# Optimization experiments

Hardware: AMD Instinct MI355X
Metric: run time of the kernel (lower is better)

## Reference

```python
import jax, jax.numpy as jnp
import numpy as np

COL_IDX = 5  # colIdx: column used as sort key
REVERSE = False


def setup_inputs() -> dict:
    key = jax.random.key(0)
    # x: [batch, seq, feat]
    x = jax.random.normal(key, (32, 4096, 256), dtype=jnp.float32)
    return {"x": x}


def reference(x):
    # tf.nn.top_k(x[:, :, nc], k=S) returns indices of a full descending sort
    # with stable tie-breaking (earlier index first). jnp.argsort is stable,
    # so argsort of the negated key reproduces it exactly.
    keys = x[:, :, COL_IDX]                       # [B, S]
    idxs = jnp.argsort(-keys, axis=1)             # [B, S] descending order
    if REVERSE:
        idxs = idxs[:, ::-1]
    # gather_nd with (batch, idx) pairs == take_along_axis over the seq dim
    return jnp.take_along_axis(x, idxs[:, :, None], axis=1)  # [B, S, F]
```

## Files before the change

kernel.cpp:

```cpp
#include <hip/hip_runtime.h>
#include <stdint.h>

#define BATCH   32
#define ROWS    4096
#define COLS    256
#define COL_IDX 5

__global__ __launch_bounds__(1024)
void sort_keys_kernel(const float* __restrict__ x, int* __restrict__ idx_out) {
    __shared__ unsigned long long keys[ROWS];
    const int b = blockIdx.x;
    const float* xb = x + (size_t)b * ROWS * COLS;

    for (int i = threadIdx.x; i < ROWS; i += blockDim.x) {
        unsigned int u = __float_as_uint(xb[(size_t)i * COLS + COL_IDX]);
        u = (u >> 31) ? ~u : (u | 0x80000000u);
        u = ~u;
        keys[i] = ((unsigned long long)u << 32) | (unsigned int)i;
    }
    __syncthreads();

    for (int k = 2; k <= ROWS; k <<= 1) {
        for (int j = k >> 1; j > 0; j >>= 1) {
            for (int i = threadIdx.x; i < ROWS; i += blockDim.x) {
                int ixj = i ^ j;
                if (ixj > i) {
                    bool up = ((i & k) == 0);
                    unsigned long long a = keys[i];
                    unsigned long long c = keys[ixj];
                    if ((a > c) == up) { keys[i] = c; keys[ixj] = a; }
                }
            }
            __syncthreads();
        }
    }

    for (int i = threadIdx.x; i < ROWS; i += blockDim.x) {
        idx_out[b * ROWS + i] = (int)(keys[i] & 0xFFFFFFFFu);
    }
}

__global__ __launch_bounds__(256)
void gather_rows_kernel(const float* __restrict__ x,
                        const int* __restrict__ idx,
                        float* __restrict__ out) {
    const int r    = blockIdx.x * 4 + (threadIdx.x >> 6);
    const int lane = threadIdx.x & 63;
    const int b    = r >> 12;
    const int src  = idx[r];

    const float4* sp = (const float4*)(x   + ((size_t)b * ROWS + src) * COLS);
    float4*       dp = (float4*)      (out + (size_t)r * COLS);
    dp[lane] = sp[lane];
}

extern "C" void kernel_launch(void* const* d_in, const int* in_sizes, int n_in,
                              void* d_out, int out_size, void* d_ws, size_t ws_size,
                              hipStream_t stream) {
    const float* x   = (const float*)d_in[0];
    float*       out = (float*)d_out;
    int*         idx = (int*)d_ws;

    sort_keys_kernel<<<BATCH, 1024, 0, stream>>>(x, idx);
    gather_rows_kernel<<<(BATCH * ROWS) / 4, 256, 0, stream>>>(x, idx, out);
}
```

Baseline: 285.8 us.

## Replace per-batch bitonic sort with parallel rank counting and scatter copy

Swaps the single-block-per-batch bitonic sort in shared memory for a rank sort. One kernel extracts the packed keys with their row indices. A second kernel has each wavefront work out every row's rank by comparing against all 4096 keys through readlane broadcasts, then scatter each source row to its ranked output position. This spreads the sort over far more wavefronts instead of 32 blocks with many barriers, at the cost of O(N^2) comparisons per batch.

```diff
diff --git a/kernel.cpp b/kernel.cpp
--- a/kernel.cpp
+++ b/kernel.cpp
@@ -6,52 +6,49 @@
 #define COLS    256
 #define COL_IDX 5
 
-__global__ __launch_bounds__(1024)
-void sort_keys_kernel(const float* __restrict__ x, int* __restrict__ idx_out) {
-    __shared__ unsigned long long keys[ROWS];
-    const int b = blockIdx.x;
-    const float* xb = x + (size_t)b * ROWS * COLS;
+typedef unsigned long long u64;
+typedef unsigned int       u32;
 
-    for (int i = threadIdx.x; i < ROWS; i += blockDim.x) {
-        unsigned int u = __float_as_uint(xb[(size_t)i * COLS + COL_IDX]);
-        u = (u >> 31) ? ~u : (u | 0x80000000u);
-        u = ~u;
-        keys[i] = ((unsigned long long)u << 32) | (unsigned int)i;
-    }
-    __syncthreads();
+__global__ __launch_bounds__(256)
+void extract_keys_kernel(const float* __restrict__ x, u64* __restrict__ keys) {
+    const int i = blockIdx.x * 256 + threadIdx.x;
+    u32 u = __float_as_uint(x[(size_t)i * COLS + COL_IDX]);
+    u = (u >> 31) ? ~u : (u | 0x80000000u);
+    u = ~u;
+    keys[i] = ((u64)u << 32) | (u32)(i & (ROWS - 1));
+}
 
-    for (int k = 2; k <= ROWS; k <<= 1) {
-        for (int j = k >> 1; j > 0; j >>= 1) {
-            for (int i = threadIdx.x; i < ROWS; i += blockDim.x) {
-                int ixj = i ^ j;
-                if (ixj > i) {
-                    bool up = ((i & k) == 0);
-                    unsigned long long a = keys[i];
-                    unsigned long long c = keys[ixj];
-                    if ((a > c) == up) { keys[i] = c; keys[ixj] = a; }
-                }
-            }
-            __syncthreads();
+__global__ __launch_bounds__(256)
+void rank_copy_kernel(const float* __restrict__ x,
+                      const u64* __restrict__ keys,
+                      float* __restrict__ out) {
+    const int wave = blockIdx.x * 4 + ((int)threadIdx.x >> 6);
+    const int lane = (int)threadIdx.x & 63;
+    const int b    = wave >> 6;
+    const int r0   = (wave & 63) << 6;
+    const u64* kb  = keys + (size_t)b * ROWS;
+
+    const u64 my = kb[r0 + lane];
+    int rank = 0;
+    for (int j0 = 0; j0 < ROWS; j0 += 64) {
+        const u64 kv = kb[j0 + lane];
+        const u32 lo = (u32)kv, hi = (u32)(kv >> 32);
+        #pragma unroll
+        for (int l = 0; l < 64; ++l) {
+            const u32 klo = (u32)__builtin_amdgcn_readlane(lo, l);
+            const u32 khi = (u32)__builtin_amdgcn_readlane(hi, l);
+            const u64 kk  = ((u64)khi << 32) | klo;
+            rank += (kk < my) ? 1 : 0;
         }
     }
 
-    for (int i = threadIdx.x; i < ROWS; i += blockDim.x) {
-        idx_out[b * ROWS + i] = (int)(keys[i] & 0xFFFFFFFFu);
+    const float4* src  = (const float4*)(x   + ((size_t)b * ROWS + r0) * COLS);
+    float4*       outb = (float4*)      (out + (size_t)b * ROWS * COLS);
+    #pragma unroll 8
+    for (int l = 0; l < 64; ++l) {
+        const int dst = __builtin_amdgcn_readlane(rank, l);
+        outb[(size_t)dst * 64 + lane] = src[l * 64 + lane];
     }
-}
-
-__global__ __launch_bounds__(256)
-void gather_rows_kernel(const float* __restrict__ x,
-                        const int* __restrict__ idx,
-                        float* __restrict__ out) {
-    const int r    = blockIdx.x * 4 + (threadIdx.x >> 6);
-    const int lane = threadIdx.x & 63;
-    const int b    = r >> 12;
-    const int src  = idx[r];
-
-    const float4* sp = (const float4*)(x   + ((size_t)b * ROWS + src) * COLS);
-    float4*       dp = (float4*)      (out + (size_t)r * COLS);
-    dp[lane] = sp[lane];
 }
 
 extern "C" void kernel_launch(void* const* d_in, const int* in_sizes, int n_in,
@@ -59,8 +56,8 @@
                               hipStream_t stream) {
     const float* x   = (const float*)d_in[0];
     float*       out = (float*)d_out;
-    int*         idx = (int*)d_ws;
+    u64*         keys = (u64*)d_ws;
 
-    sort_keys_kernel<<<BATCH, 1024, 0, stream>>>(x, idx);
-    gather_rows_kernel<<<(BATCH * ROWS) / 4, 256, 0, stream>>>(x, idx, out);
+    extract_keys_kernel<<<(BATCH * ROWS) / 256, 256, 0, stream>>>(x, keys);
+    rank_copy_kernel<<<(BATCH * ROWS) / 256, 256, 0, stream>>>(x, keys, out);
 }
```

Measured after the change: 302.6 us. 5.9% more time.
